# Optimization experiments

Measured on AMD Instinct MI355X. Metric: run time of the kernel, lower is better.

## Reference

```python
import jax, jax.numpy as jnp
import numpy as np

GROUP_SIZES = (64, 128, 256, 96, 160, 224, 192, 288, 320, 112, 80, 48, 32, 16, 32)
LENGTH = 512
ALPHABET = 21


def setup_inputs() -> dict:
    key = jax.random.key(0)
    keys = jax.random.split(key, len(GROUP_SIZES) + 1)
    n_samples = int(sum(GROUP_SIZES))
    inp = {"x": jax.random.normal(keys[0], (n_samples, LENGTH, ALPHABET), dtype=jnp.float32)}
    for i, g in enumerate(GROUP_SIZES):
        inp[f"mat{i}"] = jax.random.normal(keys[i + 1], (g, g), dtype=jnp.float32)
    return inp


def reference(x, mat0, mat1, mat2, mat3, mat4, mat5, mat6, mat7, mat8, mat9,
              mat10, mat11, mat12, mat13, mat14):
    mats = (mat0, mat1, mat2, mat3, mat4, mat5, mat6, mat7, mat8, mat9,
            mat10, mat11, mat12, mat13, mat14)
    # Block-diagonal grouped matmul along the sample dim: out[sl] = mats_i @ x[sl].
    # Group boundaries are static Python ints, so slicing is jit-friendly.
    pieces = []
    start = 0
    for m, g in zip(mats, GROUP_SIZES):
        xg = x[start:start + g]  # (g, L, A)
        pieces.append(jnp.einsum('gh,hla->gla', m, xg))
        start += g
    return jnp.concatenate(pieces, axis=0)
```

## Files before the change

### kernel.cpp

```cpp
#include <hip/hip_runtime.h>

#define NCOL 10752
#define NG 15
#define NT37 37
#define NT23 23
#define WS_NEED 913408

typedef __bf16 bf16;
typedef __attribute__((ext_vector_type(8))) __bf16 bf16x8;
typedef __attribute__((ext_vector_type(4))) __bf16 bf16x4;
typedef __attribute__((ext_vector_type(4))) float f32x4;

__constant__ int c_gsize[NG]  = {64,128,256,96,160,224,192,288,320,112,80,48,32,16,32};
__constant__ int c_gstart[NG] = {0,64,192,448,544,704,928,1120,1408,1728,1840,1920,1968,2000,2016};

__constant__ int t37_grp[NT37]  = {8,8,8,8,8, 7,7,7,7,7, 2,2,2,2, 5,5,5,5, 6,6,6, 4,4,4, 1,1, 9,9, 3,3, 10,10, 0, 11, 12, 14, 13};
__constant__ int t37_row[NT37]  = {0,64,128,192,256, 0,64,128,192,256, 0,64,128,192, 0,64,128,192, 0,64,128, 0,64,128, 0,64, 0,64, 0,64, 0,64, 0, 0, 0, 0, 0};
__constant__ int t37_kn[NT37]   = {10,10,10,10,10, 9,9,9,9,9, 8,8,8,8, 7,7,7,7, 6,6,6, 5,5,5, 4,4, 4,4, 3,3, 3,3, 2, 2, 1, 1, 1};
__constant__ int t37_base[NT37] = {0,10,20,30,40, 50,59,68,77,86, 95,103,111,119, 127,134,141,148, 155,161,167, 173,178,183, 188,192, 196,200, 204,207, 210,213, 216, 218, 220, 221, 222};

__constant__ int t23_grp[NT23] = {8,8,8,7,7,7,2,2,5,5,6,6,4,4,1,9,3,10,0,11,12,14,13};
__constant__ int t23_row[NT23] = {0,128,256,0,128,256,0,128,0,128,0,128,0,128,0,0,0,0,0,0,0,0,0};

struct MatPtrs { const float* p[NG]; };

constexpr int BKp = 40;

__device__ __forceinline__ int bkey(int col) { return ((col >> 2) & 3) << 3; }

__global__ __launch_bounds__(256)
void prep_kernel(MatPtrs mats, bf16* __restrict__ ws)
{
    const int kt = blockIdx.x, tile = blockIdx.y;
    if (kt >= t37_kn[tile]) return;
    const int grp  = t37_grp[tile];
    const int row0 = t37_row[tile];
    const int g    = c_gsize[grp];
    const float* __restrict__ M = mats.p[grp];
    bf16* dst = ws + (size_t)(t37_base[tile] + kt) * 2048;

    const int u    = threadIdx.x;
    const int l    = u & 63;
    const int st   = u >> 6;
    const int row  = row0 + st * 16 + (l & 15);
    const int kcol = kt * 32 + (l >> 4) * 8;
    bf16x8 w = {};
    if (row < g && kcol < g) {
        const float* src = M + (size_t)row * g + kcol;
        #pragma unroll
        for (int j = 0; j < 8; j++) w[j] = (bf16)src[j];
    }
    *(bf16x8*)(dst + (size_t)u * 8) = w;
}

__global__ __launch_bounds__(256, 5)
void matapply_kernel(const float* __restrict__ x, const bf16* __restrict__ aws,
                     float* __restrict__ out)
{
    __shared__ bf16 sB[4][2][32 * BKp];

    const int tid    = threadIdx.x;
    const int colb   = blockIdx.x * 128;
    const int tileid = blockIdx.y;

    const int grp  = t37_grp[tileid];
    const int g    = c_gsize[grp];
    const int s    = c_gstart[grp];
    const int row0 = t37_row[tileid];
    const int nIter = t37_kn[tileid];
    const bf16* __restrict__ aimg = aws + (size_t)t37_base[tileid] * 2048;

    const int wave = tid >> 6;
    const int lane = tid & 63;
    const int wc   = wave * 32;
    const int lm   = lane & 15;
    const int kq   = lane >> 4;
    const int kb   = kq * 8;

    const int bC = (lane & 7) * 4;
    const int bK = (lane >> 3) * 4;

    const float* __restrict__ xbase = x + (size_t)(s + bK) * NCOL + colb + wc + bC;
    bf16* __restrict__ sBw0 = &sB[wave][0][0];
    bf16* __restrict__ sBw1 = &sB[wave][1][0];

    f32x4 acc[4][2];
    #pragma unroll
    for (int i = 0; i < 4; i++) {
        acc[i][0] = (f32x4){0.f, 0.f, 0.f, 0.f};
        acc[i][1] = (f32x4){0.f, 0.f, 0.f, 0.f};
    }

    float4 xv[4];
    #pragma unroll
    for (int q = 0; q < 4; q++)
        xv[q] = *(const float4*)(xbase + (size_t)q * NCOL);

    for (int it = 0; it < nIter; ++it) {
        bf16* __restrict__ sBw = (it & 1) ? sBw1 : sBw0;

        #pragma unroll
        for (int cc = 0; cc < 4; cc++) {
            const int col = bC + cc;
            bf16x4 w;
            w[0] = (bf16)xv[0][cc]; w[1] = (bf16)xv[1][cc];
            w[2] = (bf16)xv[2][cc]; w[3] = (bf16)xv[3][cc];
            *(bf16x4*)&sBw[col * BKp + (bK ^ bkey(col))] = w;
        }

        if (it + 1 < nIter) {
            const size_t roff = (size_t)(it + 1) * 32;
            #pragma unroll
            for (int q = 0; q < 4; q++)
                xv[q] = *(const float4*)(xbase + (roff + q) * NCOL);
        }

        bf16x8 av[4];
        const bf16* ai = aimg + (size_t)it * 2048 + lane * 8;
        #pragma unroll
        for (int i = 0; i < 4; i++)
            av[i] = *(const bf16x8*)(ai + i * 512);

        bf16x8 bfr[2];
        #pragma unroll
        for (int j = 0; j < 2; j++) {
            const int col = j * 16 + lm;
            bfr[j] = *(const bf16x8*)&sBw[col * BKp + (kb ^ bkey(col))];
        }

        #pragma unroll
        for (int i = 0; i < 4; i++) {
            acc[i][0] = __builtin_amdgcn_mfma_f32_16x16x32_bf16(av[i], bfr[0], acc[i][0], 0, 0, 0);
            acc[i][1] = __builtin_amdgcn_mfma_f32_16x16x32_bf16(av[i], bfr[1], acc[i][1], 0, 0, 0);
        }
    }

    #pragma unroll
    for (int i = 0; i < 4; i++) {
        #pragma unroll
        for (int r = 0; r < 4; r++) {
            const int row = row0 + i * 16 + kq * 4 + r;
            if (row < g) {
                float* orow = out + (size_t)(s + row) * NCOL + colb + wc;
                orow[lm]      = acc[i][0][r];
                orow[16 + lm] = acc[i][1][r];
            }
        }
    }
}

__global__ __launch_bounds__(256)
void matapply_fb(const float* __restrict__ x, MatPtrs mats, float* __restrict__ out)
{
    __shared__ bf16 sAf[2][128][BKp];
    __shared__ bf16 sBf[2][128][BKp];

    const int tid    = threadIdx.x;
    const int colb   = blockIdx.x * 128;
    const int tileid = blockIdx.y;

    const int grp  = t23_grp[tileid];
    const int row0 = t23_row[tileid];
    const int g    = c_gsize[grp];
    const int s    = c_gstart[grp];
    const float* __restrict__ M = mats.p[grp];

    const int wave = tid >> 6;
    const int lane = tid & 63;
    const int wr   = (wave & 1) * 64;
    const int wc   = (wave >> 1) * 64;
    const int lm   = lane & 15;
    const int kq   = lane >> 4;
    const int kb   = kq * 8;

    const int aK = (tid & 7) * 4;
    const int aR = tid >> 3;
    const int bC = (tid & 31) * 4;
    const int bK = (tid >> 5) * 4;

    const int nIter = (g + 31) / 32;

    f32x4 acc[4][4];
    #pragma unroll
    for (int i = 0; i < 4; i++)
        #pragma unroll
        for (int j = 0; j < 4; j++)
            acc[i][j] = (f32x4){0.f, 0.f, 0.f, 0.f};

    float4 av[4], xv[4];

    #pragma unroll
    for (int i = 0; i < 4; i++) {
        int r = aR + 32 * i;
        av[i] = make_float4(0.f, 0.f, 0.f, 0.f);
        if ((row0 + r) < g && aK < g)
            av[i] = *(const float4*)(M + (size_t)(row0 + r) * g + aK);
    }
    #pragma unroll
    for (int j = 0; j < 4; j++)
        xv[j] = *(const float4*)(x + (size_t)(s + bK + j) * NCOL + colb + bC);

    #pragma unroll
    for (int i = 0; i < 4; i++) {
        int r = aR + 32 * i;
        bf16x4 w;
        w[0] = (bf16)av[i].x; w[1] = (bf16)av[i].y; w[2] = (bf16)av[i].z; w[3] = (bf16)av[i].w;
        *(bf16x4*)&sAf[0][r][aK] = w;
    }
    #pragma unroll
    for (int cc = 0; cc < 4; cc++) {
        int lc = bC + cc;
        bf16x4 w;
        #pragma unroll
        for (int j = 0; j < 4; j++)
            w[j] = (bf16)(((const float*)&xv[j])[cc]);
        *(bf16x4*)&sBf[0][lc][bK ^ (((lc >> 2) & 3) << 3)] = w;
    }
    __syncthreads();

    for (int it = 0; it < nIter; ++it) {
        const int cur = it & 1;
        const bool more = (it + 1) < nIter;

        if (more) {
            const int k0 = (it + 1) * 32;
            #pragma unroll
            for (int i = 0; i < 4; i++) {
                int r = aR + 32 * i;
                av[i] = make_float4(0.f, 0.f, 0.f, 0.f);
                if ((row0 + r) < g && (k0 + aK) < g)
                    av[i] = *(const float4*)(M + (size_t)(row0 + r) * g + k0 + aK);
            }
            #pragma unroll
            for (int j = 0; j < 4; j++)
                xv[j] = *(const float4*)(x + (size_t)(s + k0 + bK + j) * NCOL + colb + bC);
        }

        bf16x8 af[4], bfr[4];
        #pragma unroll
        for (int i = 0; i < 4; i++)
            af[i] = *(const bf16x8*)&sAf[cur][wr + i * 16 + lm][kb];
        #pragma unroll
        for (int j = 0; j < 4; j++) {
            int lc = wc + j * 16 + lm;
            bfr[j] = *(const bf16x8*)&sBf[cur][lc][kb ^ (((lc >> 2) & 3) << 3)];
        }
        #pragma unroll
        for (int i = 0; i < 4; i++)
            #pragma unroll
            for (int j = 0; j < 4; j++)
                acc[i][j] = __builtin_amdgcn_mfma_f32_16x16x32_bf16(af[i], bfr[j], acc[i][j], 0, 0, 0);

        if (more) {
            const int nxt = 1 - cur;
            #pragma unroll
            for (int i = 0; i < 4; i++) {
                int r = aR + 32 * i;
                bf16x4 w;
                w[0] = (bf16)av[i].x; w[1] = (bf16)av[i].y; w[2] = (bf16)av[i].z; w[3] = (bf16)av[i].w;
                *(bf16x4*)&sAf[nxt][r][aK] = w;
            }
            #pragma unroll
            for (int cc = 0; cc < 4; cc++) {
                int lc = bC + cc;
                bf16x4 w;
                #pragma unroll
                for (int j = 0; j < 4; j++)
                    w[j] = (bf16)(((const float*)&xv[j])[cc]);
                *(bf16x4*)&sBf[nxt][lc][bK ^ (((lc >> 2) & 3) << 3)] = w;
            }
            __syncthreads();
        }
    }

    #pragma unroll
    for (int i = 0; i < 4; i++) {
        #pragma unroll
        for (int r = 0; r < 4; r++) {
            int row = row0 + wr + i * 16 + kq * 4 + r;
            if (row < g) {
                float* orow = out + (size_t)(s + row) * NCOL + colb + wc;
                #pragma unroll
                for (int j = 0; j < 4; j++)
                    orow[j * 16 + lm] = acc[i][j][r];
            }
        }
    }
}

extern "C" void kernel_launch(void* const* d_in, const int* in_sizes, int n_in,
                              void* d_out, int out_size, void* d_ws, size_t ws_size,
                              hipStream_t stream)
{
    const float* x = (const float*)d_in[0];
    MatPtrs mp;
    for (int i = 0; i < NG; i++) mp.p[i] = (const float*)d_in[1 + i];
    float* out = (float*)d_out;

    if (d_ws != nullptr && ws_size >= (size_t)WS_NEED) {
        prep_kernel<<<dim3(10, NT37), dim3(256), 0, stream>>>(mp, (bf16*)d_ws);
        matapply_kernel<<<dim3(NCOL / 128, NT37), dim3(256), 0, stream>>>(
            x, (const bf16*)d_ws, out);
    } else {
        matapply_fb<<<dim3(NCOL / 128, NT23), dim3(256), 0, stream>>>(x, mp, out);
    }
}
```

Measured before the change: 206.6 us.

## Load B fragments directly from global into registers, dropping LDS staging

Removes the per-wave shared-memory transpose of x tiles: each lane now loads the eight K-rows it needs for the MFMA B fragment straight from global memory as scalar floats and converts them to bf16 in registers. The k-loop is unrolled by two with register double-buffering of both x and A fragments, prefetching two iterations ahead. This drops the LDS writes and reads but replaces the float4 loads with strided scalar loads, 16 per iteration per lane, and uses more registers, hence the occupancy hint lowered from 5 to 4.

```diff
diff --git a/kernel.cpp b/kernel.cpp
--- a/kernel.cpp
+++ b/kernel.cpp
@@ -25,8 +25,6 @@
 struct MatPtrs { const float* p[NG]; };
 
 constexpr int BKp = 40;
-
-__device__ __forceinline__ int bkey(int col) { return ((col >> 2) & 3) << 3; }
 
 __global__ __launch_bounds__(256)
 void prep_kernel(MatPtrs mats, bf16* __restrict__ ws)
@@ -53,20 +51,18 @@
     *(bf16x8*)(dst + (size_t)u * 8) = w;
 }
 
-__global__ __launch_bounds__(256, 5)
+__global__ __launch_bounds__(256, 4)
 void matapply_kernel(const float* __restrict__ x, const bf16* __restrict__ aws,
                      float* __restrict__ out)
 {
-    __shared__ bf16 sB[4][2][32 * BKp];
-
     const int tid    = threadIdx.x;
     const int colb   = blockIdx.x * 128;
     const int tileid = blockIdx.y;
 
-    const int grp  = t37_grp[tileid];
-    const int g    = c_gsize[grp];
-    const int s    = c_gstart[grp];
-    const int row0 = t37_row[tileid];
+    const int grp   = t37_grp[tileid];
+    const int g     = c_gsize[grp];
+    const int s     = c_gstart[grp];
+    const int row0  = t37_row[tileid];
     const int nIter = t37_kn[tileid];
     const bf16* __restrict__ aimg = aws + (size_t)t37_base[tileid] * 2048;
 
@@ -75,14 +71,9 @@
     const int wc   = wave * 32;
     const int lm   = lane & 15;
     const int kq   = lane >> 4;
-    const int kb   = kq * 8;
-
-    const int bC = (lane & 7) * 4;
-    const int bK = (lane >> 3) * 4;
-
-    const float* __restrict__ xbase = x + (size_t)(s + bK) * NCOL + colb + wc + bC;
-    bf16* __restrict__ sBw0 = &sB[wave][0][0];
-    bf16* __restrict__ sBw1 = &sB[wave][1][0];
+
+    const float* __restrict__ xp = x + (size_t)(s + kq * 8) * NCOL + colb + wc + lm;
+    const bf16*  __restrict__ ap = aimg + lane * 8;
 
     f32x4 acc[4][2];
     #pragma unroll
@@ -91,49 +82,68 @@
         acc[i][1] = (f32x4){0.f, 0.f, 0.f, 0.f};
     }
 
-    float4 xv[4];
-    #pragma unroll
-    for (int q = 0; q < 4; q++)
-        xv[q] = *(const float4*)(xbase + (size_t)q * NCOL);
-
-    for (int it = 0; it < nIter; ++it) {
-        bf16* __restrict__ sBw = (it & 1) ? sBw1 : sBw0;
-
-        #pragma unroll
-        for (int cc = 0; cc < 4; cc++) {
-            const int col = bC + cc;
-            bf16x4 w;
-            w[0] = (bf16)xv[0][cc]; w[1] = (bf16)xv[1][cc];
-            w[2] = (bf16)xv[2][cc]; w[3] = (bf16)xv[3][cc];
-            *(bf16x4*)&sBw[col * BKp + (bK ^ bkey(col))] = w;
-        }
-
-        if (it + 1 < nIter) {
-            const size_t roff = (size_t)(it + 1) * 32;
-            #pragma unroll
-            for (int q = 0; q < 4; q++)
-                xv[q] = *(const float4*)(xbase + (roff + q) * NCOL);
-        }
-
-        bf16x8 av[4];
-        const bf16* ai = aimg + (size_t)it * 2048 + lane * 8;
+    float  xf0[16], xf1[16];
+    bf16x8 avv0[4], avv1[4];
+
+    #pragma unroll
+    for (int j = 0; j < 2; j++)
+        #pragma unroll
+        for (int e = 0; e < 8; e++)
+            xf0[j * 8 + e] = xp[(size_t)e * NCOL + j * 16];
+    #pragma unroll
+    for (int i = 0; i < 4; i++)
+        avv0[i] = *(const bf16x8*)(ap + i * 512);
+    if (nIter > 1) {
+        const float* xq = xp + (size_t)32 * NCOL;
+        #pragma unroll
+        for (int j = 0; j < 2; j++)
+            #pragma unroll
+            for (int e = 0; e < 8; e++)
+                xf1[j * 8 + e] = xq[(size_t)e * NCOL + j * 16];
+        const bf16* aq = ap + 2048;
         #pragma unroll
         for (int i = 0; i < 4; i++)
-            av[i] = *(const bf16x8*)(ai + i * 512);
-
-        bf16x8 bfr[2];
-        #pragma unroll
-        for (int j = 0; j < 2; j++) {
-            const int col = j * 16 + lm;
-            bfr[j] = *(const bf16x8*)&sBw[col * BKp + (kb ^ bkey(col))];
-        }
-
-        #pragma unroll
-        for (int i = 0; i < 4; i++) {
-            acc[i][0] = __builtin_amdgcn_mfma_f32_16x16x32_bf16(av[i], bfr[0], acc[i][0], 0, 0, 0);
-            acc[i][1] = __builtin_amdgcn_mfma_f32_16x16x32_bf16(av[i], bfr[1], acc[i][1], 0, 0, 0);
-        }
-    }
+            avv1[i] = *(const bf16x8*)(aq + i * 512);
+    }
+
+    #define ITER_BODY(CUR, T)                                                  \
+    {                                                                          \
+        bf16x8 bfr[2];                                                         \
+        _Pragma("unroll")                                                      \
+        for (int j = 0; j < 2; j++) {                                          \
+            bf16x8 b;                                                          \
+            _Pragma("unroll")                                                  \
+            for (int e = 0; e < 8; e++) b[e] = (bf16)xf##CUR[j * 8 + e];       \
+            bfr[j] = b;                                                        \
+        }                                                                      \
+        if ((T) + 2 < nIter) {                                                 \
+            const float* xq = xp + (size_t)((T) + 2) * 32 * NCOL;              \
+            _Pragma("unroll")                                                  \
+            for (int j = 0; j < 2; j++)                                        \
+                _Pragma("unroll")                                              \
+                for (int e = 0; e < 8; e++)                                    \
+                    xf##CUR[j * 8 + e] = xq[(size_t)e * NCOL + j * 16];        \
+        }                                                                      \
+        _Pragma("unroll")                                                      \
+        for (int i = 0; i < 4; i++) {                                          \
+            acc[i][0] = __builtin_amdgcn_mfma_f32_16x16x32_bf16(               \
+                avv##CUR[i], bfr[0], acc[i][0], 0, 0, 0);                      \
+            acc[i][1] = __builtin_amdgcn_mfma_f32_16x16x32_bf16(               \
+                avv##CUR[i], bfr[1], acc[i][1], 0, 0, 0);                      \
+        }                                                                      \
+        if ((T) + 2 < nIter) {                                                 \
+            const bf16* aq = ap + (size_t)((T) + 2) * 2048;                    \
+            _Pragma("unroll")                                                  \
+            for (int i = 0; i < 4; i++)                                        \
+                avv##CUR[i] = *(const bf16x8*)(aq + i * 512);                  \
+        }                                                                      \
+    }
+
+    for (int t = 0; t < nIter; t += 2) {
+        ITER_BODY(0, t);
+        if (t + 1 < nIter) ITER_BODY(1, t + 1);
+    }
+    #undef ITER_BODY
 
     #pragma unroll
     for (int i = 0; i < 4; i++) {
```

After: 225.7 us. +9.2%, slower.

## Retile grouped matmul to 128x64 blocks with shared B and register-prefetched A

Applied to the files above, without the earlier changes.

Replaces the 37 row tiles of 64 rows (128 columns, private per-wave B buffers) with 23 tiles of 128 rows by 64 columns. Four waves now share one double-buffered LDS B tile, arranged as a 2x2 wave grid. The x loads are prefetched two iterations ahead and the A fragments one iteration ahead, with a block barrier per iteration. This aims to cut redundant x reads across row tiles and hide global latency, at the cost of block-wide synchronisation and a larger prep workspace.

```diff
diff --git a/kernel.cpp b/kernel.cpp
--- a/kernel.cpp
+++ b/kernel.cpp
@@ -2,87 +2,91 @@
 
 #define NCOL 10752
 #define NG 15
-#define NT37 37
-#define NT23 23
-#define WS_NEED 913408
+#define NTILES 23
+#define WS_NEED 1064960
 
 typedef __bf16 bf16;
 typedef __attribute__((ext_vector_type(8))) __bf16 bf16x8;
 typedef __attribute__((ext_vector_type(4))) __bf16 bf16x4;
+typedef __attribute__((ext_vector_type(2))) __bf16 bf16x2;
 typedef __attribute__((ext_vector_type(4))) float f32x4;
 
 __constant__ int c_gsize[NG]  = {64,128,256,96,160,224,192,288,320,112,80,48,32,16,32};
 __constant__ int c_gstart[NG] = {0,64,192,448,544,704,928,1120,1408,1728,1840,1920,1968,2000,2016};
-
-__constant__ int t37_grp[NT37]  = {8,8,8,8,8, 7,7,7,7,7, 2,2,2,2, 5,5,5,5, 6,6,6, 4,4,4, 1,1, 9,9, 3,3, 10,10, 0, 11, 12, 14, 13};
-__constant__ int t37_row[NT37]  = {0,64,128,192,256, 0,64,128,192,256, 0,64,128,192, 0,64,128,192, 0,64,128, 0,64,128, 0,64, 0,64, 0,64, 0,64, 0, 0, 0, 0, 0};
-__constant__ int t37_kn[NT37]   = {10,10,10,10,10, 9,9,9,9,9, 8,8,8,8, 7,7,7,7, 6,6,6, 5,5,5, 4,4, 4,4, 3,3, 3,3, 2, 2, 1, 1, 1};
-__constant__ int t37_base[NT37] = {0,10,20,30,40, 50,59,68,77,86, 95,103,111,119, 127,134,141,148, 155,161,167, 173,178,183, 188,192, 196,200, 204,207, 210,213, 216, 218, 220, 221, 222};
-
-__constant__ int t23_grp[NT23] = {8,8,8,7,7,7,2,2,5,5,6,6,4,4,1,9,3,10,0,11,12,14,13};
-__constant__ int t23_row[NT23] = {0,128,256,0,128,256,0,128,0,128,0,128,0,128,0,0,0,0,0,0,0,0,0};
+__constant__ int c_tgrp[NTILES]  = {8,8,8,7,7,7,2,2,5,5,6,6,4,4,1,9,3,10,0,11,12,14,13};
+__constant__ int c_trow[NTILES]  = {0,128,256,0,128,256,0,128,0,128,0,128,0,128,0,0,0,0,0,0,0,0,0};
+__constant__ int c_niter[NTILES] = {10,10,10,9,9,9,8,8,7,7,6,6,5,5,4,4,3,3,2,2,1,1,1};
+__constant__ int c_tbase[NTILES] = {0,10,20,30,39,48,57,65,73,80,87,93,99,104,109,113,117,120,123,125,127,128,129};
 
 struct MatPtrs { const float* p[NG]; };
 
 constexpr int BKp = 40;
 
-__device__ __forceinline__ int bkey(int col) { return ((col >> 2) & 3) << 3; }
+#define BAR_LGKM() do {                                   \
+    asm volatile("s_waitcnt lgkmcnt(0)" ::: "memory");    \
+    __builtin_amdgcn_sched_barrier(0);                    \
+    __builtin_amdgcn_s_barrier();                         \
+    __builtin_amdgcn_sched_barrier(0);                    \
+} while (0)
 
 __global__ __launch_bounds__(256)
 void prep_kernel(MatPtrs mats, bf16* __restrict__ ws)
 {
     const int kt = blockIdx.x, tile = blockIdx.y;
-    if (kt >= t37_kn[tile]) return;
-    const int grp  = t37_grp[tile];
-    const int row0 = t37_row[tile];
+    if (kt >= c_niter[tile]) return;
+    const int grp  = c_tgrp[tile];
+    const int row0 = c_trow[tile];
     const int g    = c_gsize[grp];
     const float* __restrict__ M = mats.p[grp];
-    bf16* dst = ws + (size_t)(t37_base[tile] + kt) * 2048;
-
-    const int u    = threadIdx.x;
-    const int l    = u & 63;
-    const int st   = u >> 6;
-    const int row  = row0 + st * 16 + (l & 15);
-    const int kcol = kt * 32 + (l >> 4) * 8;
-    bf16x8 w = {};
-    if (row < g && kcol < g) {
-        const float* src = M + (size_t)row * g + kcol;
-        #pragma unroll
-        for (int j = 0; j < 8; j++) w[j] = (bf16)src[j];
-    }
-    *(bf16x8*)(dst + (size_t)u * 8) = w;
+    bf16* dst = ws + (size_t)(c_tbase[tile] + kt) * 4096;
+
+    #pragma unroll
+    for (int h = 0; h < 2; h++) {
+        const int u    = threadIdx.x + h * 256;
+        const int l    = u & 63;
+        const int st   = u >> 6;
+        const int row  = row0 + st * 16 + (l & 15);
+        const int kcol = kt * 32 + (l >> 4) * 8;
+        bf16x8 w = {};
+        if (row < g && kcol < g) {
+            const float* src = M + (size_t)row * g + kcol;
+            #pragma unroll
+            for (int j = 0; j < 8; j++) w[j] = (bf16)src[j];
+        }
+        *(bf16x8*)(dst + (size_t)u * 8) = w;
+    }
 }
 
 __global__ __launch_bounds__(256, 5)
 void matapply_kernel(const float* __restrict__ x, const bf16* __restrict__ aws,
                      float* __restrict__ out)
 {
-    __shared__ bf16 sB[4][2][32 * BKp];
+    __shared__ bf16 sB[2][64][BKp];
 
     const int tid    = threadIdx.x;
-    const int colb   = blockIdx.x * 128;
+    const int colb   = blockIdx.x * 64;
     const int tileid = blockIdx.y;
 
-    const int grp  = t37_grp[tileid];
+    const int grp  = c_tgrp[tileid];
     const int g    = c_gsize[grp];
     const int s    = c_gstart[grp];
-    const int row0 = t37_row[tileid];
-    const int nIter = t37_kn[tileid];
-    const bf16* __restrict__ aimg = aws + (size_t)t37_base[tileid] * 2048;
+    const int row0 = c_trow[tileid];
+    const int nIter = c_niter[tileid];
+    const bf16* __restrict__ aimg = aws + (size_t)c_tbase[tileid] * 4096;
 
     const int wave = tid >> 6;
     const int lane = tid & 63;
-    const int wc   = wave * 32;
+    const int wr   = (wave & 1) * 64;
+    const int wc   = (wave >> 1) * 32;
     const int lm   = lane & 15;
     const int kq   = lane >> 4;
     const int kb   = kq * 8;
 
-    const int bC = (lane & 7) * 4;
-    const int bK = (lane >> 3) * 4;
-
-    const float* __restrict__ xbase = x + (size_t)(s + bK) * NCOL + colb + wc + bC;
-    bf16* __restrict__ sBw0 = &sB[wave][0][0];
-    bf16* __restrict__ sBw1 = &sB[wave][1][0];
+    const int bC = (tid & 15) * 4;
+    const int bK = (tid >> 4) * 2;
+
+    const float* __restrict__ xbase = x + (size_t)(s + bK) * NCOL + colb + bC;
+    const bf16* __restrict__ abase = aimg + (size_t)((wave & 1) * 4) * 512 + lane * 8;
 
     f32x4 acc[4][2];
     #pragma unroll
@@ -91,55 +95,76 @@
         acc[i][1] = (f32x4){0.f, 0.f, 0.f, 0.f};
     }
 
-    float4 xv[4];
-    #pragma unroll
-    for (int q = 0; q < 4; q++)
-        xv[q] = *(const float4*)(xbase + (size_t)q * NCOL);
+    auto stageB = [&](int buf, const float4* v) {
+        #pragma unroll
+        for (int cc = 0; cc < 4; cc++) {
+            const int lc = bC + cc;
+            bf16x2 w;
+            w[0] = (bf16)(((const float*)&v[0])[cc]);
+            w[1] = (bf16)(((const float*)&v[1])[cc]);
+            *(bf16x2*)&sB[buf][lc][bK ^ (((lc >> 2) & 3) << 3)] = w;
+        }
+    };
+
+    float4 xv[2];
+    bf16x8 av[4];
+
+    float4 xp[2];
+    #pragma unroll
+    for (int q = 0; q < 2; q++)
+        xp[q] = *(const float4*)(xbase + (size_t)q * NCOL);
+    if (nIter > 1) {
+        #pragma unroll
+        for (int q = 0; q < 2; q++)
+            xv[q] = *(const float4*)(xbase + (size_t)(32 + q) * NCOL);
+    }
+    #pragma unroll
+    for (int i = 0; i < 4; i++)
+        av[i] = *(const bf16x8*)(abase + i * 512);
+    stageB(0, xp);
+    BAR_LGKM();
 
     for (int it = 0; it < nIter; ++it) {
-        bf16* __restrict__ sBw = (it & 1) ? sBw1 : sBw0;
-
-        #pragma unroll
-        for (int cc = 0; cc < 4; cc++) {
-            const int col = bC + cc;
-            bf16x4 w;
-            w[0] = (bf16)xv[0][cc]; w[1] = (bf16)xv[1][cc];
-            w[2] = (bf16)xv[2][cc]; w[3] = (bf16)xv[3][cc];
-            *(bf16x4*)&sBw[col * BKp + (bK ^ bkey(col))] = w;
-        }
-
-        if (it + 1 < nIter) {
-            const size_t roff = (size_t)(it + 1) * 32;
-            #pragma unroll
-            for (int q = 0; q < 4; q++)
+        const int  cur = it & 1;
+        const bool w1  = (it + 1) < nIter;
+        const bool w2  = (it + 2) < nIter;
+
+        if (w1) stageB(1 - cur, xv);
+
+        if (w2) {
+            const size_t roff = (size_t)(it + 2) * 32;
+            #pragma unroll
+            for (int q = 0; q < 2; q++)
                 xv[q] = *(const float4*)(xbase + (roff + q) * NCOL);
         }
 
-        bf16x8 av[4];
-        const bf16* ai = aimg + (size_t)it * 2048 + lane * 8;
-        #pragma unroll
-        for (int i = 0; i < 4; i++)
-            av[i] = *(const bf16x8*)(ai + i * 512);
-
         bf16x8 bfr[2];
         #pragma unroll
         for (int j = 0; j < 2; j++) {
-            const int col = j * 16 + lm;
-            bfr[j] = *(const bf16x8*)&sBw[col * BKp + (kb ^ bkey(col))];
-        }
-
+            const int col = wc + j * 16 + lm;
+            bfr[j] = *(const bf16x8*)&sB[cur][col][kb ^ (((col >> 2) & 3) << 3)];
+        }
         #pragma unroll
         for (int i = 0; i < 4; i++) {
             acc[i][0] = __builtin_amdgcn_mfma_f32_16x16x32_bf16(av[i], bfr[0], acc[i][0], 0, 0, 0);
             acc[i][1] = __builtin_amdgcn_mfma_f32_16x16x32_bf16(av[i], bfr[1], acc[i][1], 0, 0, 0);
         }
+
+        if (w1) {
+            const bf16* aq = abase + (size_t)(it + 1) * 4096;
+            #pragma unroll
+            for (int i = 0; i < 4; i++)
+                av[i] = *(const bf16x8*)(aq + i * 512);
+        }
+
+        if (w1) BAR_LGKM();
     }
 
     #pragma unroll
     for (int i = 0; i < 4; i++) {
         #pragma unroll
         for (int r = 0; r < 4; r++) {
-            const int row = row0 + i * 16 + kq * 4 + r;
+            const int row = row0 + wr + i * 16 + kq * 4 + r;
             if (row < g) {
                 float* orow = out + (size_t)(s + row) * NCOL + colb + wc;
                 orow[lm]      = acc[i][0][r];
@@ -159,8 +184,8 @@
     const int colb   = blockIdx.x * 128;
     const int tileid = blockIdx.y;
 
-    const int grp  = t23_grp[tileid];
-    const int row0 = t23_row[tileid];
+    const int grp  = c_tgrp[tileid];
+    const int row0 = c_trow[tileid];
     const int g    = c_gsize[grp];
     const int s    = c_gstart[grp];
     const float* __restrict__ M = mats.p[grp];
@@ -298,10 +323,10 @@
     float* out = (float*)d_out;
 
     if (d_ws != nullptr && ws_size >= (size_t)WS_NEED) {
-        prep_kernel<<<dim3(10, NT37), dim3(256), 0, stream>>>(mp, (bf16*)d_ws);
-        matapply_kernel<<<dim3(NCOL / 128, NT37), dim3(256), 0, stream>>>(
+        prep_kernel<<<dim3(10, NTILES), dim3(256), 0, stream>>>(mp, (bf16*)d_ws);
+        matapply_kernel<<<dim3(NCOL / 64, NTILES), dim3(256), 0, stream>>>(
             x, (const bf16*)d_ws, out);
     } else {
-        matapply_fb<<<dim3(NCOL / 128, NT23), dim3(256), 0, stream>>>(x, mp, out);
+        matapply_fb<<<dim3(NCOL / 128, NTILES), dim3(256), 0, stream>>>(x, mp, out);
     }
 }
```

Measured after the change: 201.4 us. 2.5% less time.
